# Performance work log

Hardware: AMD Instinct MI355X
Metric: run time of the kernel (lower is better)

The kernel has to match this reference:

```python
import jax, jax.numpy as jnp
import numpy as np

C = 512; HEADS = 4; HD = C // HEADS
WS = (5, 9); EXP = (2, 4); FW = (5, 9)
SCALE = HD ** -0.5
B, T, NH, NW = 1, 5, 60, 108

def _valid_ind_rolled():
    wh, ww = WS; eh, ew = EXP
    tl = np.ones((wh, ww)); tl[:-eh, :-ew] = 0
    tr = np.ones((wh, ww)); tr[:-eh, ew:] = 0
    bl = np.ones((wh, ww)); bl[eh:, :-ew] = 0
    br = np.ones((wh, ww)); br[eh:, ew:] = 0
    return np.nonzero(np.stack([tl, tr, bl, br], 0).reshape(-1))[0]

VIR = jnp.asarray(_valid_ind_rolled())  # 120 valid rolled positions

def window_partition(x):
    b, t, h, w, c = x.shape
    x = x.reshape(b, t, h // WS[0], WS[0], w // WS[1], WS[1], c)
    return x.transpose(0, 2, 4, 1, 3, 5, 6).reshape(-1, t * WS[0] * WS[1], c)

def unfold(x, ker, pad):
    # torch.nn.Unfold(kernel=ker, stride=1, padding=pad): (n,c,h,w)->(n,c*kh*kw,L)
    n, c, h, w = x.shape
    xp = jnp.pad(x, ((0, 0), (0, 0), (pad[0], pad[0]), (pad[1], pad[1])))
    oh = h + 2 * pad[0] - ker[0] + 1
    ow = w + 2 * pad[1] - ker[1] + 1
    rows = jnp.arange(oh)[:, None] + jnp.arange(ker[0])[None, :]
    cols = jnp.arange(ow)[:, None] + jnp.arange(ker[1])[None, :]
    p = xp[:, :, rows[:, None, :, None], cols[None, :, None, :]]  # (n,c,oh,ow,kh,kw)
    return p.transpose(0, 1, 4, 5, 2, 3).reshape(n, c * ker[0] * ker[1], oh * ow)

def setup_inputs():
    key = jax.random.key(0)
    ks = jax.random.split(key, 4)
    return {
        "x0": jax.random.normal(ks[0], (B, T, NH, NW, C), jnp.float32),
        "x1": jax.random.normal(ks[1], (B, NH // WS[0], NW // WS[1], T, C), jnp.float32),
        "W_qkv": jax.random.normal(ks[2], (C, 3 * C), jnp.float32) * 0.02,
        "b_qkv": jnp.zeros((3 * C,), jnp.float32),
        "W_proj": jax.random.normal(ks[3], (C, C), jnp.float32) * 0.02,
        "b_proj": jnp.zeros((C,), jnp.float32),
    }

def reference(x0, x1, W_qkv, b_qkv, W_proj, b_proj):
    b, t, nh, nw, c = x0.shape
    wa = t * WS[0] * WS[1]  # tokens per window (225)
    qkv = (x0 @ W_qkv + b_qkv).reshape(b, t, nh, nw, 3, c)
    q, k, v = qkv[..., 0, :], qkv[..., 1, :], qkv[..., 2, :]

    def to_win(z):
        w = window_partition(z).reshape(-1, t, WS[0] * WS[1], HEADS, HD)
        return w.transpose(0, 3, 1, 2, 4).reshape(-1, HEADS, wa, HD)

    q_w, k_w, v_w = to_win(q), to_win(k), to_win(v)

    shifts = [(-EXP[0], -EXP[1]), (-EXP[0], EXP[1]), (EXP[0], -EXP[1]), (EXP[0], EXP[1])]
    def rolled(z):
        parts = [window_partition(jnp.roll(z, s, axis=(2, 3))).reshape(-1, t, WS[0] * WS[1], HEADS, HD) for s in shifts]
        r = jnp.concatenate(parts, axis=2).transpose(0, 3, 1, 2, 4)[:, :, :, VIR]
        return r.reshape(-1, HEADS, t * VIR.shape[0], HD)

    k_rolled = jnp.concatenate([k_w, rolled(k)], 2)
    v_rolled = jnp.concatenate([v_w, rolled(v)], 2)

    # focal level 1 pooling (focal_level=2 -> single unfold level, stride 1)
    xp = x1.transpose(0, 3, 1, 2, 4)  # (B,T,nWh,nWw,C)
    nwh, nww = xp.shape[2], xp.shape[3]
    ker = (2 * (FW[0] // 2) + 1, 2 * (FW[1] // 2) + 1)  # (5,9)
    pad = (ker[0] // 2, ker[1] // 2)
    L = nwh * nww; kk = ker[0] * ker[1]
    um = unfold(jnp.ones((t, 1, nwh, nww), x0.dtype), ker, pad)  # (T,kk,L)
    um = um.reshape(1, t, ker[0], ker[1], L).transpose(4, 1, 2, 3, 0).reshape(L, t * kk)
    pool_mask = jnp.where(um == 0, jnp.float32(-100.0), jnp.float32(0.0))  # (L, T*kk)

    qkv_p = (xp @ W_qkv + b_qkv).reshape(b, t, nwh, nww, 3, c).transpose(4, 0, 1, 5, 2, 3).reshape(3, b * t, c, nwh, nww)
    def pooled(z):
        u = unfold(z, ker, pad).reshape(b, t, c, ker[0], ker[1], L).transpose(0, 5, 1, 3, 4, 2)
        u = u.reshape(-1, t, kk, HEADS, HD).transpose(0, 3, 1, 2, 4)
        return u.reshape(-1, HEADS, t * kk, HD)

    k_all = jnp.concatenate([k_rolled, pooled(qkv_p[1])], 2)
    v_all = jnp.concatenate([v_rolled, pooled(qkv_p[2])], 2)

    attn = jnp.einsum('bhqd,bhkd->bhqk', q_w * SCALE, k_all)
    offset = k_rolled.shape[2]
    pm = jnp.tile(pool_mask[None], (b, 1, 1)).reshape(-1, t * kk)[:, None, None, :]
    attn = attn.at[:, :, :, offset:].add(pm)
    attn = jax.nn.softmax(attn, axis=-1)
    out = jnp.einsum('bhqk,bhkd->bqhd', attn, v_all).reshape(attn.shape[0], wa, c)
    return out @ W_proj + b_proj
```

## Files before the change

### kernel.cpp

```cpp
#include <hip/hip_runtime.h>

typedef _Float16 h16;
typedef __attribute__((ext_vector_type(8))) _Float16 half8;
typedef __attribute__((ext_vector_type(2))) _Float16 half2v;
typedef __attribute__((ext_vector_type(4))) float float4v;

typedef const __attribute__((address_space(1))) unsigned char gu8;
typedef __attribute__((address_space(3))) unsigned char su8;

#define NTOK  32400
#define NPTOK 720
#define CDIM  512
#define SCALE 0.08838834764831845f
#define ZROW  NTOK
#define PROW  (NTOK + 1)

__constant__ int VIR_TBL[120] = {
  5,6,7,8, 14,15,16,17, 23,24,25,26,
  27,28,29,30,31,32,33,34,35, 36,37,38,39,40,41,42,43,44,
  45,46,47,48, 54,55,56,57, 63,64,65,66,
  72,73,74,75,76,77,78,79,80, 81,82,83,84,85,86,87,88,89,
  90,91,92,93,94,95,96,97,98, 99,100,101,102,103,104,105,106,107,
  113,114,115,116, 122,123,124,125, 131,132,133,134,
  135,136,137,138,139,140,141,142,143, 144,145,146,147,148,149,150,151,152,
  153,154,155,156, 162,163,164,165, 171,172,173,174
};

__global__ __launch_bounds__(256) void build_tok(int* __restrict__ Tok,
                                                 int* __restrict__ WMask) {
  const int win = blockIdx.x;
  const int wy = win / 12, wx = win % 12;
  for (int kidx = threadIdx.x; kidx < 1056; kidx += 256) {
    int e;
    if (kidx < 225) {
      int t = kidx / 45, pos = kidx % 45;
      int y = wy * 5 + pos / 9, x = wx * 9 + pos % 9;
      e = (t * 60 + y) * 108 + x;
    } else if (kidx < 825) {
      int jj = kidx - 225;
      int t = jj / 120, m = jj % 120;
      int vir = VIR_TBL[m];
      int p = vir / 45, pos = vir % 45;
      int r = pos / 9, c = pos % 9;
      int sy = (p < 2) ? -2 : 2;
      int sx = (p & 1) ? 4 : -4;
      int y = (wy * 5 + r - sy + 60) % 60;
      int x = (wx * 9 + c - sx + 108) % 108;
      e = (t * 60 + y) * 108 + x;
    } else if (kidx < 1050) {
      int jp = kidx - 825;
      int t = jp / 45, pos = jp % 45;
      int py = wy + pos / 9 - 2;
      int px = wx + pos % 9 - 4;
      e = (py >= 0 && py < 12 && px >= 0 && px < 12)
            ? (PROW + t * 144 + py * 12 + px) : ZROW;
    } else {
      e = ZROW;
    }
    Tok[win * 1056 + kidx] = e;
  }
  if (threadIdx.x < 33) {
    int m = 0;
#pragma unroll 1
    for (int r = 0; r < 32; r++) {
      int kidx = threadIdx.x * 32 + r;
      bool v;
      if (kidx < 825) v = true;
      else if (kidx < 1050) {
        int jp = kidx - 825, pos = jp % 45;
        int py = wy + pos / 9 - 2, px = wx + pos % 9 - 4;
        v = (py >= 0 && py < 12 && px >= 0 && px < 12);
      } else v = false;
      m |= (v ? 1 : 0) << r;
    }
    WMask[win * 33 + threadIdx.x] = m;
  }
}

__global__ __launch_bounds__(256) void zero_rows(h16* __restrict__ a,
                                                 h16* __restrict__ b) {
  for (int k = threadIdx.x; k < 512; k += 256) {
    a[(size_t)ZROW * CDIM + k] = (h16)0.f;
    b[(size_t)ZROW * CDIM + k] = (h16)0.f;
  }
}

__global__ __launch_bounds__(256) void transpose_cvt(const float* __restrict__ src,
                                                     h16* __restrict__ dst,
                                                     int R, int C) {
  __shared__ float T[32][33];
  const int t = threadIdx.x;
  const int ct = blockIdx.x * 32;
  const int rt = blockIdx.y * 32;
  const int c = t & 31, r0 = (t >> 5) * 4;
#pragma unroll
  for (int i = 0; i < 4; i++)
    T[r0 + i][c] = src[(size_t)(rt + r0 + i) * C + ct + c];
  __syncthreads();
#pragma unroll
  for (int i = 0; i < 4; i++)
    dst[(size_t)(ct + r0 + i) * R + rt + c] = (h16)T[c][r0 + i];
}

__global__ __launch_bounds__(256) void cvt_x0(const float* __restrict__ src,
                                              h16* __restrict__ dst) {
  const int total = NTOK * CDIM / 8;
  for (int i = blockIdx.x * 256 + threadIdx.x; i < total; i += gridDim.x * 256) {
    const float4* s = (const float4*)(src + (size_t)i * 8);
    float4 f0 = s[0], f1 = s[1];
    half8 h;
    h[0] = (h16)f0.x; h[1] = (h16)f0.y; h[2] = (h16)f0.z; h[3] = (h16)f0.w;
    h[4] = (h16)f1.x; h[5] = (h16)f1.y; h[6] = (h16)f1.z; h[7] = (h16)f1.w;
    *(half8*)(dst + (size_t)i * 8) = h;
  }
}

struct __align__(16) StageLDS { h16 Ah[128][32]; h16 Bh[128][32]; };
union __align__(16) GemmLDS { StageLDS s; h16 Cs[128][136]; };

__global__ __launch_bounds__(256) void gemm_qkv_mfma(
    const h16* __restrict__ A, const h16* __restrict__ Bt,
    const float* __restrict__ bias,
    h16* __restrict__ Q, h16* __restrict__ K, h16* __restrict__ V)
{
  __shared__ GemmLDS u;
  const int tid = threadIdx.x;
  const int lane = tid & 63, wv = tid >> 6;
  const int col = lane & 15, quad = lane >> 4;
  const int bn = blockIdx.x, bm = blockIdx.y;
  const int mo = (wv & 1) * 64, no = (wv >> 1) * 64;

  float4v acc[4][4];
#pragma unroll
  for (int i = 0; i < 4; i++)
#pragma unroll
    for (int j = 0; j < 4; j++) acc[i][j] = (float4v){0.f, 0.f, 0.f, 0.f};

  const int lrow = lane >> 2, lcol = (lane & 3) * 8;
  const int arow = bm * 128 + wv * 32 + lrow;
  const int ar = arow < NTOK ? arow : (NTOK - 1);
  const int ar2 = (arow + 16) < NTOK ? (arow + 16) : (NTOK - 1);
  const h16* Ag  = A + (size_t)ar * 512 + lcol;
  const h16* Ag2 = A + (size_t)ar2 * 512 + lcol;
  const h16* Bg  = Bt + (size_t)(bn * 128 + wv * 32 + lrow) * 512 + lcol;
  su8* Al = (su8*)&u.s.Ah[wv * 32][0];
  su8* Bl = (su8*)&u.s.Bh[wv * 32][0];

  for (int k0 = 0; k0 < 512; k0 += 32) {
    __syncthreads();
    __builtin_amdgcn_global_load_lds((gu8*)(Ag + k0),            Al,        16, 0, 0);
    __builtin_amdgcn_global_load_lds((gu8*)(Ag2 + k0),           Al + 1024, 16, 0, 0);
    __builtin_amdgcn_global_load_lds((gu8*)(Bg + k0),            Bl,        16, 0, 0);
    __builtin_amdgcn_global_load_lds((gu8*)(Bg + k0 + 16 * 512), Bl + 1024, 16, 0, 0);
    __syncthreads();

    half8 afr[4], bfr[4];
#pragma unroll
    for (int i = 0; i < 4; i++)
      afr[i] = *(const half8*)&u.s.Ah[mo + i * 16 + col][quad * 8];
#pragma unroll
    for (int j = 0; j < 4; j++)
      bfr[j] = *(const half8*)&u.s.Bh[no + j * 16 + col][quad * 8];
#pragma unroll
    for (int i = 0; i < 4; i++)
#pragma unroll
      for (int j = 0; j < 4; j++)
        acc[i][j] = __builtin_amdgcn_mfma_f32_16x16x32_f16(afr[i], bfr[j], acc[i][j], 0, 0, 0);
  }

  __syncthreads();
  float bv[4];
#pragma unroll
  for (int j = 0; j < 4; j++) bv[j] = bias[bn * 128 + no + j * 16 + col];
#pragma unroll
  for (int i = 0; i < 4; i++)
#pragma unroll
    for (int j = 0; j < 4; j++)
#pragma unroll
      for (int r = 0; r < 4; r++)
        u.Cs[mo + i * 16 + quad * 4 + r][no + j * 16 + col] = (h16)(acc[i][j][r] + bv[j]);
  __syncthreads();

  const int row_l = tid >> 1, halfseg = (tid & 1) * 64;
  const int row_g = bm * 128 + row_l;
  const int jsel = bn >> 2;
  const int ch0 = (bn & 3) * 128 + halfseg;
  h16* dst = (jsel == 0) ? Q : (jsel == 1) ? K : V;
  if (row_g < NTOK) {
#pragma unroll
    for (int c = 0; c < 64; c += 8)
      *(half8*)&dst[(size_t)row_g * 512 + ch0 + c] = *(const half8*)&u.Cs[row_l][halfseg + c];
  }
}

__global__ __launch_bounds__(256) void gemm_proj_mfma(
    const h16* __restrict__ A, const h16* __restrict__ Bt,
    const float* __restrict__ bias, float* __restrict__ out)
{
  __shared__ StageLDS s;
  const int tid = threadIdx.x;
  const int lane = tid & 63, wv = tid >> 6;
  const int col = lane & 15, quad = lane >> 4;
  const int bn = blockIdx.x, bm = blockIdx.y;
  const int mo = (wv & 1) * 64, no = (wv >> 1) * 64;

  float4v acc[4][4];
#pragma unroll
  for (int i = 0; i < 4; i++)
#pragma unroll
    for (int j = 0; j < 4; j++) acc[i][j] = (float4v){0.f, 0.f, 0.f, 0.f};

  const int lrow = lane >> 2, lcol = (lane & 3) * 8;
  const int arow = bm * 128 + wv * 32 + lrow;
  const int ar = arow < NTOK ? arow : (NTOK - 1);
  const int ar2 = (arow + 16) < NTOK ? (arow + 16) : (NTOK - 1);
  const h16* Ag  = A + (size_t)ar * 512 + lcol;
  const h16* Ag2 = A + (size_t)ar2 * 512 + lcol;
  const h16* Bg  = Bt + (size_t)(bn * 128 + wv * 32 + lrow) * 512 + lcol;
  su8* Al = (su8*)&s.Ah[wv * 32][0];
  su8* Bl = (su8*)&s.Bh[wv * 32][0];

  for (int k0 = 0; k0 < 512; k0 += 32) {
    __syncthreads();
    __builtin_amdgcn_global_load_lds((gu8*)(Ag + k0),            Al,        16, 0, 0);
    __builtin_amdgcn_global_load_lds((gu8*)(Ag2 + k0),           Al + 1024, 16, 0, 0);
    __builtin_amdgcn_global_load_lds((gu8*)(Bg + k0),            Bl,        16, 0, 0);
    __builtin_amdgcn_global_load_lds((gu8*)(Bg + k0 + 16 * 512), Bl + 1024, 16, 0, 0);
    __syncthreads();

    half8 afr[4], bfr[4];
#pragma unroll
    for (int i = 0; i < 4; i++)
      afr[i] = *(const half8*)&s.Ah[mo + i * 16 + col][quad * 8];
#pragma unroll
    for (int j = 0; j < 4; j++)
      bfr[j] = *(const half8*)&s.Bh[no + j * 16 + col][quad * 8];
#pragma unroll
    for (int i = 0; i < 4; i++)
#pragma unroll
      for (int j = 0; j < 4; j++)
        acc[i][j] = __builtin_amdgcn_mfma_f32_16x16x32_f16(afr[i], bfr[j], acc[i][j], 0, 0, 0);
  }

  float bv[4];
#pragma unroll
  for (int j = 0; j < 4; j++) bv[j] = bias[bn * 128 + no + j * 16 + col];
#pragma unroll
  for (int i = 0; i < 4; i++) {
#pragma unroll
    for (int r = 0; r < 4; r++) {
      int row_g = bm * 128 + mo + i * 16 + quad * 4 + r;
      if (row_g < NTOK) {
#pragma unroll
        for (int j = 0; j < 4; j++)
          out[(size_t)row_g * 512 + bn * 128 + no + j * 16 + col] = acc[i][j][r] + bv[j];
      }
    }
  }
}

__global__ __launch_bounds__(256) void gemm_pooled(
    const float* __restrict__ A, const float* __restrict__ B,
    const float* __restrict__ bias,
    h16* __restrict__ Kp, h16* __restrict__ Vp)
{
  __shared__ float As[64][17];
  __shared__ float Bs[16][64];
  const int tid = threadIdx.x;
  const int bm = blockIdx.x, bn = blockIdx.y;
  const int tm = tid >> 4, tn = tid & 15;
  const int lrow = tid >> 2, lk = (tid & 3) * 4;
  const int brow = tid >> 4, bcol = (tid & 15) * 4;
  float acc[4][4] = {};
  const int orow = bm * 64 + lrow;
  int srow = 0;
  if (orow < NPTOK) { int t = orow / 144, rem = orow % 144; srow = rem * 5 + t; }
  const float* Ap = A + (size_t)srow * 512 + lk;
  const float* Bp = B + (size_t)brow * 1536 + 512 + bn * 64 + bcol;

  for (int k0 = 0; k0 < 512; k0 += 16) {
    float4 av = make_float4(0.f, 0.f, 0.f, 0.f);
    if (orow < NPTOK) av = *(const float4*)(Ap + k0);
    float4 bv = *(const float4*)(Bp + (size_t)k0 * 1536);
    As[lrow][lk + 0] = av.x; As[lrow][lk + 1] = av.y;
    As[lrow][lk + 2] = av.z; As[lrow][lk + 3] = av.w;
    *(float4*)&Bs[brow][bcol] = bv;
    __syncthreads();
#pragma unroll
    for (int kk = 0; kk < 16; kk++) {
      float a[4];
#pragma unroll
      for (int i = 0; i < 4; i++) a[i] = As[tm * 4 + i][kk];
      float4 b = *(const float4*)&Bs[kk][tn * 4];
#pragma unroll
      for (int i = 0; i < 4; i++) {
        acc[i][0] = fmaf(a[i], b.x, acc[i][0]);
        acc[i][1] = fmaf(a[i], b.y, acc[i][1]);
        acc[i][2] = fmaf(a[i], b.z, acc[i][2]);
        acc[i][3] = fmaf(a[i], b.w, acc[i][3]);
      }
    }
    __syncthreads();
  }
  const int nl = bn * 64 + tn * 4;
  const int j = nl >> 9;
  const int ch = nl & 511;
  h16* dst = (j == 0) ? Kp : Vp;
#pragma unroll
  for (int i = 0; i < 4; i++) {
    int r = bm * 64 + tm * 4 + i;
    if (r < NPTOK) {
#pragma unroll
      for (int c = 0; c < 4; c++)
        dst[(size_t)r * 512 + ch + c] = (h16)(acc[i][c] + bias[512 + nl + c]);
    }
  }
}

__global__ __launch_bounds__(256, 3) void attn_kernel(
    const h16* __restrict__ Qh, const h16* __restrict__ KhU,
    const h16* __restrict__ VhU, const int* __restrict__ Tok,
    const int* __restrict__ WMask, h16* __restrict__ AOh)
{
  __shared__ __align__(16) h16 Ks[2][32 * 136];
  __shared__ __align__(16) h16 Vt[2][128 * 40];

  const int tid = threadIdx.x;
  const int lane = tid & 63;
  const int wv = tid >> 6;
  const int win = blockIdx.x;
  const int head = blockIdx.y;
  const int qg = blockIdx.z;
  const int wy = win / 12, wx = win % 12;
  const int col = lane & 15;
  const int quad = lane >> 4;
  const int* TokW = Tok + win * 1056;
  const int* WMaskW = WMask + win * 33;

  half8 qfrag[2][4];
  const int tile0 = qg * 8 + wv * 2;
#pragma unroll
  for (int tt = 0; tt < 2; tt++) {
    int qrow = (tile0 + tt) * 16 + col;
    if (qrow < 225) {
      int t = qrow / 45, pos = qrow % 45;
      int y = wy * 5 + pos / 9, x = wx * 9 + pos % 9;
      const h16* qsrc = Qh + (size_t)((t * 60 + y) * 108 + x) * CDIM + head * 128;
#pragma unroll
      for (int dc = 0; dc < 4; dc++)
        qfrag[tt][dc] = *(const half8*)(qsrc + dc * 32 + quad * 8);
    } else {
#pragma unroll
      for (int dc = 0; dc < 4; dc++)
#pragma unroll
        for (int jj = 0; jj < 8; jj++) qfrag[tt][dc][jj] = (h16)0.f;
    }
  }

  float4v O[2][8];
#pragma unroll
  for (int tt = 0; tt < 2; tt++)
#pragma unroll
    for (int i = 0; i < 8; i++) O[tt][i] = (float4v){0.f, 0.f, 0.f, 0.f};
  float lp[2] = {0.f, 0.f};

  const int krow = tid >> 3, kseg = tid & 7;
  const int vrp = tid >> 4, vcg = tid & 15;
  const int kch = head * 128 + kseg * 16;
  const int vch = head * 128 + vcg * 8;
  const int rp = (vrp + (vcg & 3) * 4) & 15;

  {
    const h16* ks = KhU + (size_t)TokW[krow] * CDIM + kch;
    half8 k0c = *(const half8*)ks;
    half8 k1c = *(const half8*)(ks + 8);
    half8 vac = *(const half8*)(VhU + (size_t)TokW[2 * vrp] * CDIM + vch);
    half8 vbc = *(const half8*)(VhU + (size_t)TokW[2 * vrp + 1] * CDIM + vch);
    *(half8*)&Ks[0][krow * 136 + kseg * 16] = k0c;
    *(half8*)&Ks[0][krow * 136 + kseg * 16 + 8] = k1c;
#pragma unroll
    for (int i = 0; i < 8; i++) {
      half2v w; w[0] = vac[i]; w[1] = vbc[i];
      *(half2v*)&Vt[0][(vcg * 8 + i) * 40 + rp * 2] = w;
    }
  }
  half8 k0n, k1n, van, vbn;
  {
    const h16* ks = KhU + (size_t)TokW[32 + krow] * CDIM + kch;
    k0n = *(const half8*)ks;
    k1n = *(const half8*)(ks + 8);
    van = *(const half8*)(VhU + (size_t)TokW[32 + 2 * vrp] * CDIM + vch);
    vbn = *(const half8*)(VhU + (size_t)TokW[32 + 2 * vrp + 1] * CDIM + vch);
  }
  int tokK[2], tokVa[2], tokVb[2];
  tokK[0] = TokW[64 + krow]; tokVa[0] = TokW[64 + 2 * vrp]; tokVb[0] = TokW[64 + 2 * vrp + 1];
  tokK[1] = TokW[96 + krow]; tokVa[1] = TokW[96 + 2 * vrp]; tokVb[1] = TokW[96 + 2 * vrp + 1];
  __syncthreads();

  for (int step = 0; step < 33; ++step) {
    const int cur = step & 1;

    if (step + 1 < 33) {
      h16* KsN = Ks[cur ^ 1];
      h16* VtN = Vt[cur ^ 1];
      *(half8*)&KsN[krow * 136 + kseg * 16] = k0n;
      *(half8*)&KsN[krow * 136 + kseg * 16 + 8] = k1n;
#pragma unroll
      for (int i = 0; i < 8; i++) {
        half2v w; w[0] = van[i]; w[1] = vbn[i];
        *(half2v*)&VtN[(vcg * 8 + i) * 40 + rp * 2] = w;
      }
    }
    if (step + 2 < 33) {
      const h16* ks = KhU + (size_t)tokK[cur] * CDIM + kch;
      k0n = *(const half8*)ks;
      k1n = *(const half8*)(ks + 8);
      van = *(const half8*)(VhU + (size_t)tokVa[cur] * CDIM + vch);
      vbn = *(const half8*)(VhU + (size_t)tokVb[cur] * CDIM + vch);
      if (step + 4 < 33) {
        tokK[cur]  = TokW[(step + 4) * 32 + krow];
        tokVa[cur] = TokW[(step + 4) * 32 + 2 * vrp];
        tokVb[cur] = TokW[(step + 4) * 32 + 2 * vrp + 1];
      }
    }

    const int mask = WMaskW[step];
    const h16* KsC = Ks[cur];
    const h16* VtC = Vt[cur];

    float4v s0[2] = {{0.f,0.f,0.f,0.f},{0.f,0.f,0.f,0.f}};
    float4v s1[2] = {{0.f,0.f,0.f,0.f},{0.f,0.f,0.f,0.f}};
    __builtin_amdgcn_s_setprio(1);
#pragma unroll
    for (int dc = 0; dc < 4; dc++) {
      half8 a0 = *(const half8*)&KsC[col * 136 + dc * 32 + quad * 8];
      half8 a1 = *(const half8*)&KsC[(col + 16) * 136 + dc * 32 + quad * 8];
#pragma unroll
      for (int tt = 0; tt < 2; tt++) {
        s0[tt] = __builtin_amdgcn_mfma_f32_16x16x32_f16(a0, qfrag[tt][dc], s0[tt], 0, 0, 0);
        s1[tt] = __builtin_amdgcn_mfma_f32_16x16x32_f16(a1, qfrag[tt][dc], s1[tt], 0, 0, 0);
      }
    }
    __builtin_amdgcn_s_setprio(0);

    half8 pfrag[2];
    const int srcA = (((quad << 1) & 3) << 4) | col;
    const int srcB = ((((quad << 1) + 1) & 3) << 4) | col;
    const bool hi = quad >= 2;
#pragma unroll
    for (int tt = 0; tt < 2; tt++) {
      float pm0[4], pm1[4];
#pragma unroll
      for (int i = 0; i < 4; i++) {
        int r = quad * 4 + i;
        float e0 = __expf(s0[tt][i] * SCALE);
        float e1 = __expf(s1[tt][i] * SCALE);
        pm0[i] = ((mask >> r) & 1) ? e0 : 0.f;
        pm1[i] = ((mask >> (16 + r)) & 1) ? e1 : 0.f;
        lp[tt] += pm0[i] + pm1[i];
      }
      float g00 = __builtin_bit_cast(float, __builtin_amdgcn_cvt_pkrtz(pm0[0], pm0[1]));
      float g01 = __builtin_bit_cast(float, __builtin_amdgcn_cvt_pkrtz(pm0[2], pm0[3]));
      float g10 = __builtin_bit_cast(float, __builtin_amdgcn_cvt_pkrtz(pm1[0], pm1[1]));
      float g11 = __builtin_bit_cast(float, __builtin_amdgcn_cvt_pkrtz(pm1[2], pm1[3]));
      float a0 = __shfl(g00, srcA), a1 = __shfl(g01, srcA);
      float a2 = __shfl(g00, srcB), a3 = __shfl(g01, srcB);
      float b0 = __shfl(g10, srcA), b1 = __shfl(g11, srcA);
      float b2 = __shfl(g10, srcB), b3 = __shfl(g11, srcB);
      float4v pf;
      pf[0] = hi ? b0 : a0;
      pf[1] = hi ? b1 : a1;
      pf[2] = hi ? b2 : a2;
      pf[3] = hi ? b3 : a3;
      pfrag[tt] = __builtin_bit_cast(half8, pf);
    }

    __builtin_amdgcn_s_setprio(1);
#pragma unroll
    for (int dt = 0; dt < 8; dt++) {
      int ch = dt * 16 + col;
      int g4 = ((dt * 2 + (col >> 3)) & 3) * 4;
      int x0 = (quad * 4 + g4) & 15;
      half8 vf = *(const half8*)&VtC[ch * 40 + x0 * 2];
#pragma unroll
      for (int tt = 0; tt < 2; tt++)
        O[tt][dt] = __builtin_amdgcn_mfma_f32_16x16x32_f16(pfrag[tt], vf, O[tt][dt], 0, 0, 0);
    }
    __builtin_amdgcn_s_setprio(0);

    __syncthreads();
  }

#pragma unroll
  for (int tt = 0; tt < 2; tt++) {
    float l_all = lp[tt];
    l_all += __shfl_xor(l_all, 16);
    l_all += __shfl_xor(l_all, 32);
#pragma unroll
    for (int i = 0; i < 4; i++) {
      int qr = (tile0 + tt) * 16 + quad * 4 + i;
      if (qr < 225) {
        float invl = __builtin_amdgcn_rcpf(__shfl(l_all, quad * 4 + i));
        h16* dst = AOh + ((size_t)win * 225 + qr) * CDIM + head * 128 + col;
#pragma unroll
        for (int dt = 0; dt < 8; dt++)
          dst[dt * 16] = (h16)(O[tt][dt][i] * invl);
      }
    }
  }
}

extern "C" void kernel_launch(void* const* d_in, const int* in_sizes, int n_in,
                              void* d_out, int out_size, void* d_ws, size_t ws_size,
                              hipStream_t stream) {
  const float* x0    = (const float*)d_in[0];
  const float* x1    = (const float*)d_in[1];
  const float* Wqkv  = (const float*)d_in[2];
  const float* bqkv  = (const float*)d_in[3];
  const float* Wproj = (const float*)d_in[4];
  const float* bproj = (const float*)d_in[5];
  float* out = (float*)d_out;

  const size_t NU = (size_t)(NTOK + 1 + NPTOK);
  h16* Qh   = (h16*)d_ws;
  h16* KhU  = Qh + (size_t)NTOK * CDIM;
  h16* VhU  = KhU + NU * CDIM;
  h16* Rh   = VhU + NU * CDIM;
  h16* Wqkvt  = Rh + (size_t)NTOK * CDIM;
  h16* Wprojt = Wqkvt + (size_t)1536 * 512;
  int* Tok    = (int*)(Wprojt + (size_t)512 * 512);
  int* WMaskP = Tok + (size_t)144 * 1056;

  build_tok<<<144, 256, 0, stream>>>(Tok, WMaskP);
  zero_rows<<<1, 256, 0, stream>>>(KhU, VhU);
  transpose_cvt<<<dim3(48, 16), 256, 0, stream>>>(Wqkv, Wqkvt, 512, 1536);
  transpose_cvt<<<dim3(16, 16), 256, 0, stream>>>(Wproj, Wprojt, 512, 512);
  cvt_x0<<<2048, 256, 0, stream>>>(x0, Rh);

  gemm_qkv_mfma<<<dim3(12, 254), 256, 0, stream>>>(Rh, Wqkvt, bqkv, Qh, KhU, VhU);
  gemm_pooled<<<dim3(12, 16), 256, 0, stream>>>(x1, Wqkv, bqkv,
                                                KhU + (size_t)PROW * CDIM,
                                                VhU + (size_t)PROW * CDIM);
  attn_kernel<<<dim3(144, 4, 2), 256, 0, stream>>>(Qh, KhU, VhU, Tok, WMaskP, Rh);
  gemm_proj_mfma<<<dim3(4, 254), 256, 0, stream>>>(Rh, Wprojt, bproj, out);
}
```

Before: 458.2 us.

## Double-buffer GEMM LDS tiles and merge attention query groups into one block

```diff
diff --git a/kernel.cpp b/kernel.cpp
--- a/kernel.cpp
+++ b/kernel.cpp
@@ -2,6 +2,7 @@
 
 typedef _Float16 h16;
 typedef __attribute__((ext_vector_type(8))) _Float16 half8;
+typedef __attribute__((ext_vector_type(4))) _Float16 half4;
 typedef __attribute__((ext_vector_type(2))) _Float16 half2v;
 typedef __attribute__((ext_vector_type(4))) float float4v;
 
@@ -115,15 +116,15 @@
   }
 }
 
-struct __align__(16) StageLDS { h16 Ah[128][32]; h16 Bh[128][32]; };
-union __align__(16) GemmLDS { StageLDS s; h16 Cs[128][136]; };
+struct __align__(16) Stage2 { h16 Ah[2][128][32]; h16 Bh[2][128][32]; };
+union __align__(16) GemmLDSQ { Stage2 s; h16 Cs[128][136]; };
 
 __global__ __launch_bounds__(256) void gemm_qkv_mfma(
     const h16* __restrict__ A, const h16* __restrict__ Bt,
     const float* __restrict__ bias,
     h16* __restrict__ Q, h16* __restrict__ K, h16* __restrict__ V)
 {
-  __shared__ GemmLDS u;
+  __shared__ GemmLDSQ u;
   const int tid = threadIdx.x;
   const int lane = tid & 63, wv = tid >> 6;
   const int col = lane & 15, quad = lane >> 4;
@@ -143,32 +144,37 @@
   const h16* Ag  = A + (size_t)ar * 512 + lcol;
   const h16* Ag2 = A + (size_t)ar2 * 512 + lcol;
   const h16* Bg  = Bt + (size_t)(bn * 128 + wv * 32 + lrow) * 512 + lcol;
-  su8* Al = (su8*)&u.s.Ah[wv * 32][0];
-  su8* Bl = (su8*)&u.s.Bh[wv * 32][0];
-
-  for (int k0 = 0; k0 < 512; k0 += 32) {
-    __syncthreads();
-    __builtin_amdgcn_global_load_lds((gu8*)(Ag + k0),            Al,        16, 0, 0);
-    __builtin_amdgcn_global_load_lds((gu8*)(Ag2 + k0),           Al + 1024, 16, 0, 0);
-    __builtin_amdgcn_global_load_lds((gu8*)(Bg + k0),            Bl,        16, 0, 0);
-    __builtin_amdgcn_global_load_lds((gu8*)(Bg + k0 + 16 * 512), Bl + 1024, 16, 0, 0);
-    __syncthreads();
+
+#define STAGE_G(buf, k0) do {                                              \
+    su8* Al = (su8*)&u.s.Ah[buf][wv * 32][0];                              \
+    su8* Bl = (su8*)&u.s.Bh[buf][wv * 32][0];                              \
+    __builtin_amdgcn_global_load_lds((gu8*)(Ag + (k0)),            Al,        16, 0, 0); \
+    __builtin_amdgcn_global_load_lds((gu8*)(Ag2 + (k0)),           Al + 1024, 16, 0, 0); \
+    __builtin_amdgcn_global_load_lds((gu8*)(Bg + (k0)),            Bl,        16, 0, 0); \
+    __builtin_amdgcn_global_load_lds((gu8*)(Bg + (k0) + 16 * 512), Bl + 1024, 16, 0, 0); \
+  } while (0)
+
+  STAGE_G(0, 0);
+  __syncthreads();
+  for (int kt = 0; kt < 16; kt++) {
+    const int cur = kt & 1;
+    if (kt + 1 < 16) STAGE_G(cur ^ 1, (kt + 1) * 32);
 
     half8 afr[4], bfr[4];
 #pragma unroll
     for (int i = 0; i < 4; i++)
-      afr[i] = *(const half8*)&u.s.Ah[mo + i * 16 + col][quad * 8];
+      afr[i] = *(const half8*)&u.s.Ah[cur][mo + i * 16 + col][quad * 8];
 #pragma unroll
     for (int j = 0; j < 4; j++)
-      bfr[j] = *(const half8*)&u.s.Bh[no + j * 16 + col][quad * 8];
+      bfr[j] = *(const half8*)&u.s.Bh[cur][no + j * 16 + col][quad * 8];
 #pragma unroll
     for (int i = 0; i < 4; i++)
 #pragma unroll
       for (int j = 0; j < 4; j++)
         acc[i][j] = __builtin_amdgcn_mfma_f32_16x16x32_f16(afr[i], bfr[j], acc[i][j], 0, 0, 0);
-  }
-
-  __syncthreads();
+    __syncthreads();
+  }
+
   float bv[4];
 #pragma unroll
   for (int j = 0; j < 4; j++) bv[j] = bias[bn * 128 + no + j * 16 + col];
@@ -197,7 +203,7 @@
     const h16* __restrict__ A, const h16* __restrict__ Bt,
     const float* __restrict__ bias, float* __restrict__ out)
 {
-  __shared__ StageLDS s;
+  __shared__ Stage2 s;
   const int tid = threadIdx.x;
   const int lane = tid & 63, wv = tid >> 6;
   const int col = lane & 15, quad = lane >> 4;
@@ -217,29 +223,35 @@
   const h16* Ag  = A + (size_t)ar * 512 + lcol;
   const h16* Ag2 = A + (size_t)ar2 * 512 + lcol;
   const h16* Bg  = Bt + (size_t)(bn * 128 + wv * 32 + lrow) * 512 + lcol;
-  su8* Al = (su8*)&s.Ah[wv * 32][0];
-  su8* Bl = (su8*)&s.Bh[wv * 32][0];
-
-  for (int k0 = 0; k0 < 512; k0 += 32) {
-    __syncthreads();
-    __builtin_amdgcn_global_load_lds((gu8*)(Ag + k0),            Al,        16, 0, 0);
-    __builtin_amdgcn_global_load_lds((gu8*)(Ag2 + k0),           Al + 1024, 16, 0, 0);
-    __builtin_amdgcn_global_load_lds((gu8*)(Bg + k0),            Bl,        16, 0, 0);
-    __builtin_amdgcn_global_load_lds((gu8*)(Bg + k0 + 16 * 512), Bl + 1024, 16, 0, 0);
-    __syncthreads();
+
+#define STAGE_P(buf, k0) do {                                              \
+    su8* Al = (su8*)&s.Ah[buf][wv * 32][0];                                \
+    su8* Bl = (su8*)&s.Bh[buf][wv * 32][0];                                \
+    __builtin_amdgcn_global_load_lds((gu8*)(Ag + (k0)),            Al,        16, 0, 0); \
+    __builtin_amdgcn_global_load_lds((gu8*)(Ag2 + (k0)),           Al + 1024, 16, 0, 0); \
+    __builtin_amdgcn_global_load_lds((gu8*)(Bg + (k0)),            Bl,        16, 0, 0); \
+    __builtin_amdgcn_global_load_lds((gu8*)(Bg + (k0) + 16 * 512), Bl + 1024, 16, 0, 0); \
+  } while (0)
+
+  STAGE_P(0, 0);
+  __syncthreads();
+  for (int kt = 0; kt < 16; kt++) {
+    const int cur = kt & 1;
+    if (kt + 1 < 16) STAGE_P(cur ^ 1, (kt + 1) * 32);
 
     half8 afr[4], bfr[4];
 #pragma unroll
     for (int i = 0; i < 4; i++)
-      afr[i] = *(const half8*)&s.Ah[mo + i * 16 + col][quad * 8];
+      afr[i] = *(const half8*)&s.Ah[cur][mo + i * 16 + col][quad * 8];
 #pragma unroll
     for (int j = 0; j < 4; j++)
-      bfr[j] = *(const half8*)&s.Bh[no + j * 16 + col][quad * 8];
+      bfr[j] = *(const half8*)&s.Bh[cur][no + j * 16 + col][quad * 8];
 #pragma unroll
     for (int i = 0; i < 4; i++)
 #pragma unroll
       for (int j = 0; j < 4; j++)
         acc[i][j] = __builtin_amdgcn_mfma_f32_16x16x32_f16(afr[i], bfr[j], acc[i][j], 0, 0, 0);
+    __syncthreads();
   }
 
   float bv[4];
@@ -317,7 +329,7 @@
   }
 }
 
-__global__ __launch_bounds__(256, 3) void attn_kernel(
+__global__ __launch_bounds__(512, 2) void attn_kernel(
     const h16* __restrict__ Qh, const h16* __restrict__ KhU,
     const h16* __restrict__ VhU, const int* __restrict__ Tok,
     const int* __restrict__ WMask, h16* __restrict__ AOh)
@@ -330,7 +342,6 @@
   const int wv = tid >> 6;
   const int win = blockIdx.x;
   const int head = blockIdx.y;
-  const int qg = blockIdx.z;
   const int wy = win / 12, wx = win % 12;
   const int col = lane & 15;
   const int quad = lane >> 4;
@@ -338,7 +349,7 @@
   const int* WMaskW = WMask + win * 33;
 
   half8 qfrag[2][4];
-  const int tile0 = qg * 8 + wv * 2;
+  const int tile0 = wv * 2;
 #pragma unroll
   for (int tt = 0; tt < 2; tt++) {
     int qrow = (tile0 + tt) * 16 + col;
@@ -364,34 +375,27 @@
     for (int i = 0; i < 8; i++) O[tt][i] = (float4v){0.f, 0.f, 0.f, 0.f};
   float lp[2] = {0.f, 0.f};
 
-  const int krow = tid >> 3, kseg = tid & 7;
-  const int vrp = tid >> 4, vcg = tid & 15;
-  const int kch = head * 128 + kseg * 16;
-  const int vch = head * 128 + vcg * 8;
-  const int rp = (vrp + (vcg & 3) * 4) & 15;
+  const int krow = tid >> 4, kseg = tid & 15;
+  const int vrp  = tid >> 5, vcg6 = tid & 31;
+  const int kch = head * 128 + kseg * 8;
+  const int vch = head * 128 + vcg6 * 4;
+  const int rp  = (vrp + ((vcg6 >> 1) & 3) * 4) & 15;
 
   {
-    const h16* ks = KhU + (size_t)TokW[krow] * CDIM + kch;
-    half8 k0c = *(const half8*)ks;
-    half8 k1c = *(const half8*)(ks + 8);
-    half8 vac = *(const half8*)(VhU + (size_t)TokW[2 * vrp] * CDIM + vch);
-    half8 vbc = *(const half8*)(VhU + (size_t)TokW[2 * vrp + 1] * CDIM + vch);
-    *(half8*)&Ks[0][krow * 136 + kseg * 16] = k0c;
-    *(half8*)&Ks[0][krow * 136 + kseg * 16 + 8] = k1c;
-#pragma unroll
-    for (int i = 0; i < 8; i++) {
-      half2v w; w[0] = vac[i]; w[1] = vbc[i];
-      *(half2v*)&Vt[0][(vcg * 8 + i) * 40 + rp * 2] = w;
-    }
-  }
-  half8 k0n, k1n, van, vbn;
-  {
-    const h16* ks = KhU + (size_t)TokW[32 + krow] * CDIM + kch;
-    k0n = *(const half8*)ks;
-    k1n = *(const half8*)(ks + 8);
-    van = *(const half8*)(VhU + (size_t)TokW[32 + 2 * vrp] * CDIM + vch);
-    vbn = *(const half8*)(VhU + (size_t)TokW[32 + 2 * vrp + 1] * CDIM + vch);
-  }
+    half8 kc = *(const half8*)(KhU + (size_t)TokW[krow] * CDIM + kch);
+    half4 va = *(const half4*)(VhU + (size_t)TokW[2 * vrp] * CDIM + vch);
+    half4 vb = *(const half4*)(VhU + (size_t)TokW[2 * vrp + 1] * CDIM + vch);
+    *(half8*)&Ks[0][krow * 136 + kseg * 8] = kc;
+#pragma unroll
+    for (int i = 0; i < 4; i++) {
+      half2v w; w[0] = va[i]; w[1] = vb[i];
+      *(half2v*)&Vt[0][(vcg6 * 4 + i) * 40 + rp * 2] = w;
+    }
+  }
+  half8 kn; half4 van, vbn;
+  kn  = *(const half8*)(KhU + (size_t)TokW[32 + krow] * CDIM + kch);
+  van = *(const half4*)(VhU + (size_t)TokW[32 + 2 * vrp] * CDIM + vch);
+  vbn = *(const half4*)(VhU + (size_t)TokW[32 + 2 * vrp + 1] * CDIM + vch);
   int tokK[2], tokVa[2], tokVb[2];
   tokK[0] = TokW[64 + krow]; tokVa[0] = TokW[64 + 2 * vrp]; tokVb[0] = TokW[64 + 2 * vrp + 1];
   tokK[1] = TokW[96 + krow]; tokVa[1] = TokW[96 + 2 * vrp]; tokVb[1] = TokW[96 + 2 * vrp + 1];
@@ -401,22 +405,18 @@
     const int cur = step & 1;
 
     if (step + 1 < 33) {
-      h16* KsN = Ks[cur ^ 1];
+      *(half8*)&Ks[cur ^ 1][krow * 136 + kseg * 8] = kn;
       h16* VtN = Vt[cur ^ 1];
-      *(half8*)&KsN[krow * 136 + kseg * 16] = k0n;
-      *(half8*)&KsN[krow * 136 + kseg * 16 + 8] = k1n;
-#pragma unroll
-      for (int i = 0; i < 8; i++) {
+#pragma unroll
+      for (int i = 0; i < 4; i++) {
         half2v w; w[0] = van[i]; w[1] = vbn[i];
-        *(half2v*)&VtN[(vcg * 8 + i) * 40 + rp * 2] = w;
+        *(half2v*)&VtN[(vcg6 * 4 + i) * 40 + rp * 2] = w;
       }
     }
     if (step + 2 < 33) {
-      const h16* ks = KhU + (size_t)tokK[cur] * CDIM + kch;
-      k0n = *(const half8*)ks;
-      k1n = *(const half8*)(ks + 8);
-      van = *(const half8*)(VhU + (size_t)tokVa[cur] * CDIM + vch);
-      vbn = *(const half8*)(VhU + (size_t)tokVb[cur] * CDIM + vch);
+      kn  = *(const half8*)(KhU + (size_t)tokK[cur] * CDIM + kch);
+      van = *(const half4*)(VhU + (size_t)tokVa[cur] * CDIM + vch);
+      vbn = *(const half4*)(VhU + (size_t)tokVb[cur] * CDIM + vch);
       if (step + 4 < 33) {
         tokK[cur]  = TokW[(step + 4) * 32 + krow];
         tokVa[cur] = TokW[(step + 4) * 32 + 2 * vrp];
@@ -541,6 +541,6 @@
   gemm_pooled<<<dim3(12, 16), 256, 0, stream>>>(x1, Wqkv, bqkv,
                                                 KhU + (size_t)PROW * CDIM,
                                                 VhU + (size_t)PROW * CDIM);
-  attn_kernel<<<dim3(144, 4, 2), 256, 0, stream>>>(Qh, KhU, VhU, Tok, WMaskP, Rh);
+  attn_kernel<<<dim3(144, 4), 512, 0, stream>>>(Qh, KhU, VhU, Tok, WMaskP, Rh);
   gemm_proj_mfma<<<dim3(4, 254), 256, 0, stream>>>(Rh, Wprojt, bproj, out);
 }
```

After: 488.5 us. +6.6%, slower.

## Double-buffer GEMM LDS staging and XOR-swizzle GEMM and attention K tiles

Applied to the files above, without the earlier changes.

```diff
diff --git a/kernel.cpp b/kernel.cpp
--- a/kernel.cpp
+++ b/kernel.cpp
@@ -115,15 +115,15 @@
   }
 }
 
-struct __align__(16) StageLDS { h16 Ah[128][32]; h16 Bh[128][32]; };
-union __align__(16) GemmLDS { StageLDS s; h16 Cs[128][136]; };
+struct __align__(16) Stage2 { h16 Ah[2][128][32]; h16 Bh[2][128][32]; };
+union __align__(16) GemmLDSQ { Stage2 s; h16 Cs[128][136]; };
 
 __global__ __launch_bounds__(256) void gemm_qkv_mfma(
     const h16* __restrict__ A, const h16* __restrict__ Bt,
     const float* __restrict__ bias,
     h16* __restrict__ Q, h16* __restrict__ K, h16* __restrict__ V)
 {
-  __shared__ GemmLDS u;
+  __shared__ GemmLDSQ u;
   const int tid = threadIdx.x;
   const int lane = tid & 63, wv = tid >> 6;
   const int col = lane & 15, quad = lane >> 4;
@@ -136,39 +136,46 @@
 #pragma unroll
     for (int j = 0; j < 4; j++) acc[i][j] = (float4v){0.f, 0.f, 0.f, 0.f};
 
-  const int lrow = lane >> 2, lcol = (lane & 3) * 8;
+  const int lrow = lane >> 2;
+  const int lcol = (((lane & 3) ^ ((lane >> 3) & 3)) * 8);
   const int arow = bm * 128 + wv * 32 + lrow;
   const int ar = arow < NTOK ? arow : (NTOK - 1);
   const int ar2 = (arow + 16) < NTOK ? (arow + 16) : (NTOK - 1);
   const h16* Ag  = A + (size_t)ar * 512 + lcol;
   const h16* Ag2 = A + (size_t)ar2 * 512 + lcol;
   const h16* Bg  = Bt + (size_t)(bn * 128 + wv * 32 + lrow) * 512 + lcol;
-  su8* Al = (su8*)&u.s.Ah[wv * 32][0];
-  su8* Bl = (su8*)&u.s.Bh[wv * 32][0];
-
-  for (int k0 = 0; k0 < 512; k0 += 32) {
-    __syncthreads();
-    __builtin_amdgcn_global_load_lds((gu8*)(Ag + k0),            Al,        16, 0, 0);
-    __builtin_amdgcn_global_load_lds((gu8*)(Ag2 + k0),           Al + 1024, 16, 0, 0);
-    __builtin_amdgcn_global_load_lds((gu8*)(Bg + k0),            Bl,        16, 0, 0);
-    __builtin_amdgcn_global_load_lds((gu8*)(Bg + k0 + 16 * 512), Bl + 1024, 16, 0, 0);
-    __syncthreads();
+
+#define STAGE_G(buf, k0) do {                                              \
+    su8* Al = (su8*)&u.s.Ah[buf][wv * 32][0];                              \
+    su8* Bl = (su8*)&u.s.Bh[buf][wv * 32][0];                              \
+    __builtin_amdgcn_global_load_lds((gu8*)(Ag + (k0)),            Al,        16, 0, 0); \
+    __builtin_amdgcn_global_load_lds((gu8*)(Ag2 + (k0)),           Al + 1024, 16, 0, 0); \
+    __builtin_amdgcn_global_load_lds((gu8*)(Bg + (k0)),            Bl,        16, 0, 0); \
+    __builtin_amdgcn_global_load_lds((gu8*)(Bg + (k0) + 16 * 512), Bl + 1024, 16, 0, 0); \
+  } while (0)
+
+  const int fsw = (quad ^ ((col >> 1) & 3)) * 8;
+  STAGE_G(0, 0);
+  __syncthreads();
+  for (int kt = 0; kt < 16; kt++) {
+    const int cur = kt & 1;
+    if (kt + 1 < 16) STAGE_G(cur ^ 1, (kt + 1) * 32);
 
     half8 afr[4], bfr[4];
 #pragma unroll
     for (int i = 0; i < 4; i++)
-      afr[i] = *(const half8*)&u.s.Ah[mo + i * 16 + col][quad * 8];
+      afr[i] = *(const half8*)&u.s.Ah[cur][mo + i * 16 + col][fsw];
 #pragma unroll
     for (int j = 0; j < 4; j++)
-      bfr[j] = *(const half8*)&u.s.Bh[no + j * 16 + col][quad * 8];
+      bfr[j] = *(const half8*)&u.s.Bh[cur][no + j * 16 + col][fsw];
 #pragma unroll
     for (int i = 0; i < 4; i++)
 #pragma unroll
       for (int j = 0; j < 4; j++)
         acc[i][j] = __builtin_amdgcn_mfma_f32_16x16x32_f16(afr[i], bfr[j], acc[i][j], 0, 0, 0);
-  }
-
-  __syncthreads();
+    __syncthreads();
+  }
+
   float bv[4];
 #pragma unroll
   for (int j = 0; j < 4; j++) bv[j] = bias[bn * 128 + no + j * 16 + col];
@@ -197,7 +204,7 @@
     const h16* __restrict__ A, const h16* __restrict__ Bt,
     const float* __restrict__ bias, float* __restrict__ out)
 {
-  __shared__ StageLDS s;
+  __shared__ Stage2 s;
   const int tid = threadIdx.x;
   const int lane = tid & 63, wv = tid >> 6;
   const int col = lane & 15, quad = lane >> 4;
@@ -210,36 +217,44 @@
 #pragma unroll
     for (int j = 0; j < 4; j++) acc[i][j] = (float4v){0.f, 0.f, 0.f, 0.f};
 
-  const int lrow = lane >> 2, lcol = (lane & 3) * 8;
+  const int lrow = lane >> 2;
+  const int lcol = (((lane & 3) ^ ((lane >> 3) & 3)) * 8);
   const int arow = bm * 128 + wv * 32 + lrow;
   const int ar = arow < NTOK ? arow : (NTOK - 1);
   const int ar2 = (arow + 16) < NTOK ? (arow + 16) : (NTOK - 1);
   const h16* Ag  = A + (size_t)ar * 512 + lcol;
   const h16* Ag2 = A + (size_t)ar2 * 512 + lcol;
   const h16* Bg  = Bt + (size_t)(bn * 128 + wv * 32 + lrow) * 512 + lcol;
-  su8* Al = (su8*)&s.Ah[wv * 32][0];
-  su8* Bl = (su8*)&s.Bh[wv * 32][0];
-
-  for (int k0 = 0; k0 < 512; k0 += 32) {
-    __syncthreads();
-    __builtin_amdgcn_global_load_lds((gu8*)(Ag + k0),            Al,        16, 0, 0);
-    __builtin_amdgcn_global_load_lds((gu8*)(Ag2 + k0),           Al + 1024, 16, 0, 0);
-    __builtin_amdgcn_global_load_lds((gu8*)(Bg + k0),            Bl,        16, 0, 0);
-    __builtin_amdgcn_global_load_lds((gu8*)(Bg + k0 + 16 * 512), Bl + 1024, 16, 0, 0);
-    __syncthreads();
+
+#define STAGE_P(buf, k0) do {                                              \
+    su8* Al = (su8*)&s.Ah[buf][wv * 32][0];                                \
+    su8* Bl = (su8*)&s.Bh[buf][wv * 32][0];                                \
+    __builtin_amdgcn_global_load_lds((gu8*)(Ag + (k0)),            Al,        16, 0, 0); \
+    __builtin_amdgcn_global_load_lds((gu8*)(Ag2 + (k0)),           Al + 1024, 16, 0, 0); \
+    __builtin_amdgcn_global_load_lds((gu8*)(Bg + (k0)),            Bl,        16, 0, 0); \
+    __builtin_amdgcn_global_load_lds((gu8*)(Bg + (k0) + 16 * 512), Bl + 1024, 16, 0, 0); \
+  } while (0)
+
+  const int fsw = (quad ^ ((col >> 1) & 3)) * 8;
+  STAGE_P(0, 0);
+  __syncthreads();
+  for (int kt = 0; kt < 16; kt++) {
+    const int cur = kt & 1;
+    if (kt + 1 < 16) STAGE_P(cur ^ 1, (kt + 1) * 32);
 
     half8 afr[4], bfr[4];
 #pragma unroll
     for (int i = 0; i < 4; i++)
-      afr[i] = *(const half8*)&s.Ah[mo + i * 16 + col][quad * 8];
+      afr[i] = *(const half8*)&s.Ah[cur][mo + i * 16 + col][fsw];
 #pragma unroll
     for (int j = 0; j < 4; j++)
-      bfr[j] = *(const half8*)&s.Bh[no + j * 16 + col][quad * 8];
+      bfr[j] = *(const half8*)&s.Bh[cur][no + j * 16 + col][fsw];
 #pragma unroll
     for (int i = 0; i < 4; i++)
 #pragma unroll
       for (int j = 0; j < 4; j++)
         acc[i][j] = __builtin_amdgcn_mfma_f32_16x16x32_f16(afr[i], bfr[j], acc[i][j], 0, 0, 0);
+    __syncthreads();
   }
 
   float bv[4];
@@ -322,7 +337,7 @@
     const h16* __restrict__ VhU, const int* __restrict__ Tok,
     const int* __restrict__ WMask, h16* __restrict__ AOh)
 {
-  __shared__ __align__(16) h16 Ks[2][32 * 136];
+  __shared__ __align__(16) h16 Ks[2][32 * 128];
   __shared__ __align__(16) h16 Vt[2][128 * 40];
 
   const int tid = threadIdx.x;
@@ -369,6 +384,8 @@
   const int kch = head * 128 + kseg * 16;
   const int vch = head * 128 + vcg * 8;
   const int rp = (vrp + (vcg & 3) * 4) & 15;
+  const int kg0 = ((2 * kseg) ^ (krow & 7)) * 8;
+  const int kg1 = ((2 * kseg + 1) ^ (krow & 7)) * 8;
 
   {
     const h16* ks = KhU + (size_t)TokW[krow] * CDIM + kch;
@@ -376,8 +393,8 @@
     half8 k1c = *(const half8*)(ks + 8);
     half8 vac = *(const half8*)(VhU + (size_t)TokW[2 * vrp] * CDIM + vch);
     half8 vbc = *(const half8*)(VhU + (size_t)TokW[2 * vrp + 1] * CDIM + vch);
-    *(half8*)&Ks[0][krow * 136 + kseg * 16] = k0c;
-    *(half8*)&Ks[0][krow * 136 + kseg * 16 + 8] = k1c;
+    *(half8*)&Ks[0][krow * 128 + kg0] = k0c;
+    *(half8*)&Ks[0][krow * 128 + kg1] = k1c;
 #pragma unroll
     for (int i = 0; i < 8; i++) {
       half2v w; w[0] = vac[i]; w[1] = vbc[i];
@@ -403,8 +420,8 @@
     if (step + 1 < 33) {
       h16* KsN = Ks[cur ^ 1];
       h16* VtN = Vt[cur ^ 1];
-      *(half8*)&KsN[krow * 136 + kseg * 16] = k0n;
-      *(half8*)&KsN[krow * 136 + kseg * 16 + 8] = k1n;
+      *(half8*)&KsN[krow * 128 + kg0] = k0n;
+      *(half8*)&KsN[krow * 128 + kg1] = k1n;
 #pragma unroll
       for (int i = 0; i < 8; i++) {
         half2v w; w[0] = van[i]; w[1] = vbn[i];
@@ -433,8 +450,9 @@
     __builtin_amdgcn_s_setprio(1);
 #pragma unroll
     for (int dc = 0; dc < 4; dc++) {
-      half8 a0 = *(const half8*)&KsC[col * 136 + dc * 32 + quad * 8];
-      half8 a1 = *(const half8*)&KsC[(col + 16) * 136 + dc * 32 + quad * 8];
+      const int kg = ((dc * 4 + quad) ^ (col & 7)) * 8;
+      half8 a0 = *(const half8*)&KsC[col * 128 + kg];
+      half8 a1 = *(const half8*)&KsC[(col + 16) * 128 + kg];
 #pragma unroll
       for (int tt = 0; tt < 2; tt++) {
         s0[tt] = __builtin_amdgcn_mfma_f32_16x16x32_f16(a0, qfrag[tt][dc], s0[tt], 0, 0, 0);
```

Result: slower. 467.4 us (+2.0%).
